# Kernel tuning notes

Hardware: AMD Instinct MI355X
Metric: run time of the kernel (lower is better)

The kernel has to match this reference:

```python
import jax, jax.numpy as jnp
import numpy as np

STATE_LEN = 128
SEQ_LEN = 2048
NUM_ITERS = 2
DIM_IN = 1024
DIM_H = 64
BATCH = 2
T_TOTAL = SEQ_LEN + 2 * STATE_LEN  # 2304
NEG = -1e30  # large-negative causal mask (avoids -inf NaNs under autodiff)


def _ln(x, g, b):
    m = jnp.mean(x, axis=-1, keepdims=True)
    v = jnp.var(x, axis=-1, keepdims=True)
    return (x - m) / jnp.sqrt(v + 1e-5) * g + b


def setup_inputs() -> dict:
    key = jax.random.key(0)
    ks = jax.random.split(key, 16)

    def w(k, fi, fo):
        # torch nn.Linear-style fan-in scaled init (keeps logits O(1))
        return jax.random.normal(k, (fi, fo), jnp.float32) / np.sqrt(fi)

    return {
        "x": jax.random.normal(ks[0], (BATCH, T_TOTAL, DIM_IN), jnp.float32),
        "Wh": w(ks[1], DIM_IN, DIM_H),
        "Whs": w(ks[2], DIM_IN, DIM_H),
        "Whe": w(ks[3], DIM_IN, DIM_H),
        "Wk": w(ks[4], DIM_H, DIM_H),
        "Wq": w(ks[5], DIM_H, DIM_H),
        "Wv": w(ks[6], DIM_H, DIM_H),
        "Wks": w(ks[7], DIM_H, DIM_H),
        "Wqs": w(ks[8], DIM_H, DIM_H),
        "Wvs": w(ks[9], DIM_H, DIM_H),
        "Wke": w(ks[10], DIM_H, DIM_H),
        "Wqe": w(ks[11], DIM_H, DIM_H),
        "Wve": w(ks[12], DIM_H, DIM_H),
        "ln_g": jnp.ones((DIM_IN,), jnp.float32),
        "ln_b": jnp.zeros((DIM_IN,), jnp.float32),
        "ln_gs": jnp.ones((DIM_IN,), jnp.float32),
        "ln_bs": jnp.zeros((DIM_IN,), jnp.float32),
        "ln_ge": jnp.ones((DIM_IN,), jnp.float32),
        "ln_be": jnp.zeros((DIM_IN,), jnp.float32),
        "cope_emb": jax.random.normal(ks[13], (DIM_H, T_TOTAL), jnp.float32),
    }


def reference(x, Wh, Whs, Whe, Wk, Wq, Wv, Wks, Wqs, Wvs, Wke, Wqe, Wve,
              ln_g, ln_b, ln_gs, ln_bs, ln_ge, ln_be, cope_emb):
    S = STATE_LEN
    # extract_state: [state_start | seq | state_end] along token dim
    xs, xm, xe = x[:, :S], x[:, S:-S], x[:, -S:]
    xm = _ln(xm, ln_g, ln_b)
    xs = _ln(xs, ln_gs, ln_bs)
    xe = _ln(xe, ln_ge, ln_be)

    mem = xm @ Wh                 # (B, L, D)
    mem_s = xs @ Whs              # (B, S, D)
    mem_e = xe @ Whe              # (B, S, D)

    scale = 1.0 / np.sqrt(DIM_H)  # xformers default scale (beta=None)
    tril = jnp.tril(jnp.ones((T_TOTAL, T_TOTAL), bool))
    mask = jnp.where(tril, 0.0, NEG)  # log of lower-triangular ones

    mem_full = None
    for ix in range(NUM_ITERS):
        k = jnp.concatenate([mem_s @ Wks, mem @ Wk, mem_e @ Wke], axis=1)  # (B,T,D)
        q = jnp.concatenate([mem_s @ Wqs, mem @ Wq, mem_e @ Wqe], axis=1)
        v = jnp.concatenate([mem_s @ Wvs, mem @ Wv, mem_e @ Wve], axis=1)

        logits = jnp.einsum('btd,bsd->bts', q, k)  # unscaled, as in CoPE gates
        if ix == 0:
            # CoPE: sigmoid-gated reverse cumsum positions + interpolated embedding bias
            gates = jax.nn.sigmoid(logits)
            pos = jnp.flip(jnp.cumsum(jnp.flip(gates, -1), axis=-1), -1)
            pos = jnp.minimum(pos, float(T_TOTAL - 1))
            pos_floor = jnp.floor(pos)
            pos_ceil = jnp.ceil(pos)
            logits_int = jnp.einsum('btd,dn->btn', q, cope_emb)  # (B,T,T)
            lc = jnp.take_along_axis(logits_int, pos_ceil.astype(jnp.int32), axis=-1)
            lf = jnp.take_along_axis(logits_int, pos_floor.astype(jnp.int32), axis=-1)
            wfrac = pos - pos_floor
            bias = lc * wfrac + lf * (1.0 - wfrac)
            scores = logits * scale + mask + bias
        else:
            scores = logits * scale + mask

        attn = jax.nn.softmax(scores, axis=-1)
        mem_full = jnp.einsum('bts,bsd->btd', attn, v)  # (B,T,D)
        if ix < NUM_ITERS - 1:
            mem_s, mem, mem_e = mem_full[:, :S], mem_full[:, S:-S], mem_full[:, -S:]
    return mem_full
```

## Files before the change

### kernel.cpp

```cpp
#include <hip/hip_runtime.h>

#define T_TOT 2304
#define S_LEN 128
#define D_IN  1024
#define D_H   64
#define BATCH 2
#define NROW  (BATCH * T_TOT)
#define CH    (T_TOT / 256)
#define SCALE 0.125f
#define KCHUNKS 8
#define KCW   (D_IN / KCHUNKS)
#define TB    16
#define FCH   288
#define NSC   8
#define NTBLK (T_TOT / TB)
#define NT16  (T_TOT / 16)
#define NPART (NSC * 4)

typedef unsigned short u16;
typedef __attribute__((ext_vector_type(8))) short short8;
typedef __attribute__((ext_vector_type(4))) float f32x4;
typedef __attribute__((ext_vector_type(4))) unsigned short u16x4;

static __device__ __forceinline__ u16 f2bf(float f) {
    unsigned u = __float_as_uint(f);
    unsigned r = (u + 0x7fffu + ((u >> 16) & 1u)) >> 16;
    return (u16)r;
}
static __device__ __forceinline__ float bf2f(u16 s) {
    return __uint_as_float((unsigned)s << 16);
}

__global__ __launch_bounds__(256) void k_ln(
    const float* __restrict__ x,
    const float* __restrict__ ln_g,  const float* __restrict__ ln_b,
    const float* __restrict__ ln_gs, const float* __restrict__ ln_bs,
    const float* __restrict__ ln_ge, const float* __restrict__ ln_be,
    u16* __restrict__ xn_hi, u16* __restrict__ xn_lo)
{
    __shared__ float red1[256], red2[256];
    const int row = blockIdx.x;
    const int t = row % T_TOT;
    const int tid = threadIdx.x;

    const float *gg, *bb;
    if (t < S_LEN)               { gg = ln_gs; bb = ln_bs; }
    else if (t >= T_TOT - S_LEN) { gg = ln_ge; bb = ln_be; }
    else                         { gg = ln_g;  bb = ln_b;  }

    const float4 xv = *(const float4*)(x + (size_t)row * D_IN + 4 * tid);
    float s  = xv.x + xv.y + xv.z + xv.w;
    float s2 = xv.x * xv.x + xv.y * xv.y + xv.z * xv.z + xv.w * xv.w;
    red1[tid] = s; red2[tid] = s2; __syncthreads();
    for (int off = 128; off > 0; off >>= 1) {
        if (tid < off) { red1[tid] += red1[tid + off]; red2[tid] += red2[tid + off]; }
        __syncthreads();
    }
    const float mean = red1[0] * (1.f / D_IN);
    const float var  = red2[0] * (1.f / D_IN) - mean * mean;
    const float rstd = rsqrtf(var + 1e-5f);

    const float4 gv = *(const float4*)(gg + 4 * tid);
    const float4 bv = *(const float4*)(bb + 4 * tid);
    float o0 = (xv.x - mean) * rstd * gv.x + bv.x;
    float o1 = (xv.y - mean) * rstd * gv.y + bv.y;
    float o2 = (xv.z - mean) * rstd * gv.z + bv.z;
    float o3 = (xv.w - mean) * rstd * gv.w + bv.w;

    u16x4 hv, lv;
    hv[0] = f2bf(o0); lv[0] = f2bf(o0 - bf2f(hv[0]));
    hv[1] = f2bf(o1); lv[1] = f2bf(o1 - bf2f(hv[1]));
    hv[2] = f2bf(o2); lv[2] = f2bf(o2 - bf2f(hv[2]));
    hv[3] = f2bf(o3); lv[3] = f2bf(o3 - bf2f(hv[3]));
    *(u16x4*)(xn_hi + (size_t)row * D_IN + 4 * tid) = hv;
    *(u16x4*)(xn_lo + (size_t)row * D_IN + 4 * tid) = lv;
}

#define WPREP_N (3 * D_H * D_IN)
__global__ __launch_bounds__(256) void k_prep(
    const float* __restrict__ Wh, const float* __restrict__ Whs, const float* __restrict__ Whe,
    const float* __restrict__ cope,
    u16* __restrict__ wT_hi, u16* __restrict__ wT_lo,
    u16* __restrict__ cT_hi, u16* __restrict__ cT_lo)
{
    const int gid = blockIdx.x * 256 + threadIdx.x;
    if (gid < WPREP_N) {
        const int seg = gid >> 16;
        const int o = gid & 65535;
        const int j = o >> 10, k = o & 1023;
        const float* W = seg == 0 ? Wh : (seg == 1 ? Whs : Whe);
        const float f = W[k * D_H + j];
        const u16 hi = f2bf(f);
        wT_hi[gid] = hi;
        wT_lo[gid] = f2bf(f - bf2f(hi));
    } else {
        const int idx = gid - WPREP_N;
        if (idx < T_TOT * D_H) {
            const int n = idx >> 6, d = idx & 63;
            const float f = cope[(size_t)d * T_TOT + n];
            const u16 hi = f2bf(f);
            cT_hi[idx] = hi;
            cT_lo[idx] = f2bf(f - bf2f(hi));
        }
    }
}

__global__ __launch_bounds__(256) void k_hgemm(
    const u16* __restrict__ xn_hi, const u16* __restrict__ xn_lo,
    const u16* __restrict__ wT_hi, const u16* __restrict__ wT_lo,
    float* __restrict__ h_part)
{
    const int tile = blockIdx.x;
    const int kc   = blockIdx.y;
    const int k0   = kc * KCW;
    const int tt = tile % 36;
    const int seg = tt < 2 ? 1 : (tt >= 34 ? 2 : 0);

    __shared__ u16 Bh[64 * KCW];
    __shared__ u16 Bl[64 * KCW];

    const int tid = threadIdx.x;
    {
        const int r = tid >> 2;
        const int c0 = (tid & 3) * 32;
        const u16* sh = wT_hi + ((size_t)seg * D_H + r) * D_IN + k0 + c0;
        const u16* sl = wT_lo + ((size_t)seg * D_H + r) * D_IN + k0 + c0;
        const int sw = (r & 7) << 3;
        #pragma unroll
        for (int u = 0; u < 4; ++u) {
            const int col = c0 + 8 * u;
            *(short8*)&Bh[r * KCW + (col ^ sw)] = *(const short8*)(sh + 8 * u);
            *(short8*)&Bl[r * KCW + (col ^ sw)] = *(const short8*)(sl + 8 * u);
        }
    }
    __syncthreads();

    const int w = tid >> 6;
    const int lane = tid & 63;
    const int l15 = lane & 15, lg4 = lane >> 4;
    const int row0 = tile * 64 + w * 16;

    const size_t abase = (size_t)(row0 + l15) * D_IN + k0 + 8 * lg4;
    f32x4 acc[4] = {};

    #pragma unroll
    for (int kk = 0; kk < KCW / 32; ++kk) {
        short8 ah = *(const short8*)(xn_hi + abase + kk * 32);
        short8 al = *(const short8*)(xn_lo + abase + kk * 32);
        #pragma unroll
        for (int j = 0; j < 4; ++j) {
            const int brow = j * 16 + l15;
            const int col = (kk * 32 + 8 * lg4) ^ ((brow & 7) << 3);
            short8 bh = *(const short8*)&Bh[brow * KCW + col];
            short8 bl = *(const short8*)&Bl[brow * KCW + col];
            acc[j] = __builtin_amdgcn_mfma_f32_16x16x32_bf16(al, bh, acc[j], 0, 0, 0);
            acc[j] = __builtin_amdgcn_mfma_f32_16x16x32_bf16(ah, bl, acc[j], 0, 0, 0);
            acc[j] = __builtin_amdgcn_mfma_f32_16x16x32_bf16(ah, bh, acc[j], 0, 0, 0);
        }
    }
    float* hp = h_part + (size_t)kc * ((size_t)NROW * D_H);
    #pragma unroll
    for (int j = 0; j < 4; ++j)
        #pragma unroll
        for (int r = 0; r < 4; ++r)
            hp[(size_t)(row0 + 4 * lg4 + r) * D_H + j * 16 + l15] = acc[j][r];
}

__global__ __launch_bounds__(256) void k_hred(
    const float* __restrict__ h_part, float* __restrict__ h)
{
    const size_t idx = (size_t)blockIdx.x * 256 + threadIdx.x;
    const size_t N = (size_t)NROW * D_H;
    float s = 0.f;
    #pragma unroll
    for (int kc = 0; kc < KCHUNKS; ++kc) s += h_part[kc * N + idx];
    h[idx] = s;
}

template <bool SPLIT>
__global__ __launch_bounds__(192) void k_qkv(
    const float* __restrict__ hin,
    const float* __restrict__ Wk,  const float* __restrict__ Wq,  const float* __restrict__ Wv,
    const float* __restrict__ Wks, const float* __restrict__ Wqs, const float* __restrict__ Wvs,
    const float* __restrict__ Wke, const float* __restrict__ Wqe, const float* __restrict__ Wve,
    u16* __restrict__ q_hi, u16* __restrict__ q_lo,
    u16* __restrict__ k_hi, u16* __restrict__ k_lo,
    u16* __restrict__ vT)
{
    __shared__ float hr[D_H];
    const int bid = blockIdx.x;
    const int b = bid / T_TOT, t = bid % T_TOT;
    const int tid = threadIdx.x;

    const float* hrow = hin + ((size_t)b * T_TOT + t) * D_H;
    if (tid < D_H) hr[tid] = hrow[tid];
    __syncthreads();

    const int which = tid >> 6, j = tid & 63;
    const float* W;
    if (t < S_LEN)               W = which == 0 ? Wks : (which == 1 ? Wqs : Wvs);
    else if (t >= T_TOT - S_LEN) W = which == 0 ? Wke : (which == 1 ? Wqe : Wve);
    else                         W = which == 0 ? Wk  : (which == 1 ? Wq  : Wv);

    float acc = 0.f;
    #pragma unroll
    for (int d = 0; d < D_H; ++d) acc += hr[d] * W[d * D_H + j];

    const size_t idx = ((size_t)b * T_TOT + t) * D_H + j;
    u16 hi = f2bf(acc);
    if (which == 0) {
        k_hi[idx] = hi;
        if (SPLIT) k_lo[idx] = f2bf(acc - bf2f(hi));
    } else if (which == 1) {
        q_hi[idx] = hi;
        if (SPLIT) q_lo[idx] = f2bf(acc - bf2f(hi));
    } else {
        vT[((size_t)b * D_H + j) * T_TOT + t] = hi;
    }
}

__global__ __launch_bounds__(256) void k_score2c(
    const u16* __restrict__ a_hi, const u16* __restrict__ a_lo,
    const u16* __restrict__ k_hi, const u16* __restrict__ k_lo,
    const u16* __restrict__ c_hi, const u16* __restrict__ c_lo,
    float* __restrict__ logits, float* __restrict__ lint,
    float* __restrict__ csum)
{
    const int b  = blockIdx.z;
    const int s0 = blockIdx.x * 64;
    const int wid = threadIdx.x >> 6;
    const int t0 = blockIdx.y * 64 + wid * 16;
    const int wt_max = t0 + 15;
    const int lane = threadIdx.x & 63;
    const int l15 = lane & 15, lg4 = lane >> 4;

    const size_t a_off = ((size_t)(b * T_TOT + t0 + l15)) * D_H + 8 * lg4;
    const short8 ah0 = *(const short8*)(a_hi + a_off);
    const short8 ah1 = *(const short8*)(a_hi + a_off + 32);
    const short8 al0 = *(const short8*)(a_lo + a_off);
    const short8 al1 = *(const short8*)(a_lo + a_off + 32);

    const size_t orow_off = ((size_t)(b * T_TOT + t0 + 4 * lg4)) * T_TOT + s0 + l15;

    {
        float* o = lint + orow_off;
        #pragma unroll
        for (int ni = 0; ni < 4; ++ni) {
            const size_t b_off = ((size_t)(s0 + ni * 16 + l15)) * D_H + 8 * lg4;
            short8 bh0 = *(const short8*)(c_hi + b_off);
            short8 bh1 = *(const short8*)(c_hi + b_off + 32);
            short8 bl0 = *(const short8*)(c_lo + b_off);
            short8 bl1 = *(const short8*)(c_lo + b_off + 32);
            f32x4 acc = {0.f, 0.f, 0.f, 0.f};
            acc = __builtin_amdgcn_mfma_f32_16x16x32_bf16(al0, bh0, acc, 0, 0, 0);
            acc = __builtin_amdgcn_mfma_f32_16x16x32_bf16(al1, bh1, acc, 0, 0, 0);
            acc = __builtin_amdgcn_mfma_f32_16x16x32_bf16(ah0, bl0, acc, 0, 0, 0);
            acc = __builtin_amdgcn_mfma_f32_16x16x32_bf16(ah1, bl1, acc, 0, 0, 0);
            acc = __builtin_amdgcn_mfma_f32_16x16x32_bf16(ah0, bh0, acc, 0, 0, 0);
            acc = __builtin_amdgcn_mfma_f32_16x16x32_bf16(ah1, bh1, acc, 0, 0, 0);
            #pragma unroll
            for (int r = 0; r < 4; ++r)
                o[(size_t)r * T_TOT + ni * 16] = acc[r];
        }
    }

    {
        const u16* bh = k_hi + (size_t)b * (T_TOT * D_H);
        const u16* bl = k_lo + (size_t)b * (T_TOT * D_H);
        float* o = logits + orow_off;
        #pragma unroll
        for (int ni = 0; ni < 4; ++ni) {
            const size_t b_off = ((size_t)(s0 + ni * 16 + l15)) * D_H + 8 * lg4;
            short8 bh0 = *(const short8*)(bh + b_off);
            short8 bh1 = *(const short8*)(bh + b_off + 32);
            short8 bl0 = *(const short8*)(bl + b_off);
            short8 bl1 = *(const short8*)(bl + b_off + 32);
            f32x4 acc = {0.f, 0.f, 0.f, 0.f};
            acc = __builtin_amdgcn_mfma_f32_16x16x32_bf16(al0, bh0, acc, 0, 0, 0);
            acc = __builtin_amdgcn_mfma_f32_16x16x32_bf16(al1, bh1, acc, 0, 0, 0);
            acc = __builtin_amdgcn_mfma_f32_16x16x32_bf16(ah0, bl0, acc, 0, 0, 0);
            acc = __builtin_amdgcn_mfma_f32_16x16x32_bf16(ah1, bl1, acc, 0, 0, 0);
            acc = __builtin_amdgcn_mfma_f32_16x16x32_bf16(ah0, bh0, acc, 0, 0, 0);
            acc = __builtin_amdgcn_mfma_f32_16x16x32_bf16(ah1, bh1, acc, 0, 0, 0);
            const int c16 = (s0 >> 4) + ni;
            #pragma unroll
            for (int r = 0; r < 4; ++r) {
                float g = 1.f / (1.f + __expf(-acc[r]));
                g += __shfl_xor(g, 1); g += __shfl_xor(g, 2);
                g += __shfl_xor(g, 4); g += __shfl_xor(g, 8);
                if (l15 == 0)
                    csum[((size_t)(b * T_TOT + t0 + 4 * lg4 + r)) * NT16 + c16] = g;
            }
            if (s0 + ni * 16 <= wt_max) {
                #pragma unroll
                for (int r = 0; r < 4; ++r)
                    o[(size_t)r * T_TOT + ni * 16] = acc[r];
            }
        }
    }
}

__global__ __launch_bounds__(256) void k_csum(
    const float* __restrict__ csum, float* __restrict__ totalv)
{
    const int row = blockIdx.x * 4 + (threadIdx.x >> 6);
    const int lane = threadIdx.x & 63;
    const size_t base = (size_t)row * NT16;
    float v = csum[base + lane] + csum[base + 64 + lane];
    if (128 + lane < NT16) v += csum[base + 128 + lane];
    #pragma unroll
    for (int off = 32; off > 0; off >>= 1) v += __shfl_xor(v, off);
    if (lane == 0) totalv[row] = v;
}

__global__ __launch_bounds__(256) void k_erow(
    const float* __restrict__ logits,
    const float* __restrict__ lint,
    const float* __restrict__ totalv,
    float* __restrict__ pbase)
{
    __shared__ float lg[T_TOT];
    __shared__ float extra[2 * T_TOT];
    __shared__ float wtot[4], wmax[4], wsum[4];

    const int row = blockIdx.x;
    const int t = row % T_TOT;
    const int Lt16 = (t | 15) + 1;
    const int Lw = min((Lt16 + 31) & ~31, T_TOT);
    const int tid = threadIdx.x;
    const int lane = tid & 63, wid = tid >> 6;
    const float* lrow = logits + (size_t)row * T_TOT;
    const float tot = totalv[row];
    const int Lc = min((int)tot + 2, T_TOT);

    for (int s = tid; s < Lt16; s += 256) lg[s] = lrow[s];
    {
        const float* lintrow = lint + (size_t)row * T_TOT;
        for (int s = tid; s < Lc; s += 256) extra[T_TOT + s] = lintrow[s];
    }
    __syncthreads();

    {
        const int base = tid * CH;
        float gv[CH];
        float lsum = 0.f;
        #pragma unroll
        for (int u = 0; u < CH; ++u) {
            const int s = base + u;
            float g = (s <= t) ? 1.f / (1.f + expf(-lg[s])) : 0.f;
            gv[u] = g;
            lsum += g;
        }
        float cs = lsum;
        #pragma unroll
        for (int off = 1; off < 64; off <<= 1) {
            float n = __shfl_up(cs, off);
            if (lane >= off) cs += n;
        }
        if (lane == 63) wtot[wid] = cs;
        __syncthreads();
        float pre = 0.f;
        #pragma unroll
        for (int w = 0; w < 4; ++w) {
            float vv = wtot[w];
            if (w < wid) pre += vv;
        }
        float run = pre + cs - lsum;
        #pragma unroll
        for (int u = 0; u < CH; ++u) {
            const int s = base + u;
            if (s <= t) {
                float p = fminf(fmaxf(tot - run, 0.f), (float)(T_TOT - 1));
                extra[s] = p;
            }
            run += gv[u];
        }
        __syncthreads();
    }

    float scv[CH];
    float mx = -3.4e38f;
    #pragma unroll
    for (int r = 0; r < CH; ++r) {
        int sidx = tid + 256 * r;
        float sc = -3.4e38f;
        if (sidx <= t) {
            sc = lg[sidx] * SCALE;
            float p = extra[sidx];
            float pf = floorf(p);
            int fi = (int)pf;
            int ci = (int)ceilf(p);
            float w = p - pf;
            sc += extra[T_TOT + ci] * w + extra[T_TOT + fi] * (1.f - w);
            mx = fmaxf(mx, sc);
        }
        scv[r] = sc;
    }
    #pragma unroll
    for (int off = 32; off > 0; off >>= 1) mx = fmaxf(mx, __shfl_xor(mx, off));
    if (lane == 0) wmax[wid] = mx;
    __syncthreads();
    mx = fmaxf(fmaxf(wmax[0], wmax[1]), fmaxf(wmax[2], wmax[3]));

    float pvv[CH];
    float psum = 0.f;
    #pragma unroll
    for (int r = 0; r < CH; ++r) {
        int sidx = tid + 256 * r;
        float pv = 0.f;
        if (sidx <= t) { pv = expf(scv[r] - mx); psum += pv; }
        pvv[r] = pv;
    }
    #pragma unroll
    for (int off = 32; off > 0; off >>= 1) psum += __shfl_xor(psum, off);
    if (lane == 0) wsum[wid] = psum;
    __syncthreads();
    const float inv = 1.f / (wsum[0] + wsum[1] + wsum[2] + wsum[3]);

    u16* prow = (u16*)(pbase + (size_t)row * T_TOT);
    #pragma unroll
    for (int r = 0; r < CH; ++r) {
        int sidx = tid + 256 * r;
        if (sidx < Lw) prow[sidx] = f2bf(pvv[r] * inv);
    }
}

__global__ __launch_bounds__(256) void k_pv(
    const float* __restrict__ pbuf, const u16* __restrict__ vT,
    float* __restrict__ opart)
{
    const int b  = blockIdx.z;
    const int scn = blockIdx.y;
    const int bx = blockIdx.x;
    const int t0 = bx * 16;
    const int sstart = scn * FCH;
    const int send = min(sstart + FCH, t0 + 16);
    if (sstart >= send) return;

    const int j0 = (threadIdx.x >> 6) * 16;
    const int lane = threadIdx.x & 63;
    const int l15 = lane & 15, lg4 = lane >> 4;

    const u16* pb = (const u16*)pbuf
        + ((size_t)(b * T_TOT + t0 + l15)) * (2 * (size_t)T_TOT) + 8 * lg4;
    const u16* vb = vT + ((size_t)(b * D_H + j0 + l15)) * T_TOT + 8 * lg4;

    f32x4 a0 = {}, a1 = {}, a2 = {}, a3 = {};
    int s = sstart;
    for (; s + 128 <= send; s += 128) {
        short8 p0 = *(const short8*)(pb + s);
        short8 v0 = *(const short8*)(vb + s);
        short8 p1 = *(const short8*)(pb + s + 32);
        short8 v1 = *(const short8*)(vb + s + 32);
        short8 p2 = *(const short8*)(pb + s + 64);
        short8 v2 = *(const short8*)(vb + s + 64);
        short8 p3 = *(const short8*)(pb + s + 96);
        short8 v3 = *(const short8*)(vb + s + 96);
        a0 = __builtin_amdgcn_mfma_f32_16x16x32_bf16(p0, v0, a0, 0, 0, 0);
        a1 = __builtin_amdgcn_mfma_f32_16x16x32_bf16(p1, v1, a1, 0, 0, 0);
        a2 = __builtin_amdgcn_mfma_f32_16x16x32_bf16(p2, v2, a2, 0, 0, 0);
        a3 = __builtin_amdgcn_mfma_f32_16x16x32_bf16(p3, v3, a3, 0, 0, 0);
    }
    for (; s < send; s += 32) {
        short8 p0 = *(const short8*)(pb + s);
        short8 v0 = *(const short8*)(vb + s);
        a0 = __builtin_amdgcn_mfma_f32_16x16x32_bf16(p0, v0, a0, 0, 0, 0);
    }
    f32x4 acc = (a0 + a1) + (a2 + a3);
    float* ob = opart + (((size_t)(b * NTBLK + bx)) * NSC + scn) * (TB * D_H)
              + (size_t)(4 * lg4) * D_H + j0 + l15;
    #pragma unroll
    for (int r = 0; r < 4; ++r) ob[(size_t)r * D_H] = acc[r];
}

__global__ __launch_bounds__(256) void k_pvmerge(
    const float* __restrict__ opart, float* __restrict__ outp)
{
    const int bid = blockIdx.x;
    const int b = bid / NTBLK, bx = bid % NTBLK;
    const int t0 = bx * 16, t_max = t0 + 15;
    const int tid = threadIdx.x;
    const int tl = tid >> 4, j4 = (tid & 15) * 4;

    float4 acc = {0.f, 0.f, 0.f, 0.f};
    for (int scn = 0; scn < NSC; ++scn) {
        if (scn * FCH <= t_max) {
            const float4 v = *(const float4*)&opart[
                (((size_t)(b * NTBLK + bx)) * NSC + scn) * (TB * D_H) + tl * D_H + j4];
            acc.x += v.x; acc.y += v.y; acc.z += v.z; acc.w += v.w;
        }
    }
    *(float4*)&outp[((size_t)(b * T_TOT + t0 + tl)) * D_H + j4] = acc;
}

__global__ __launch_bounds__(256) void k_fattn1s(
    const u16* __restrict__ q_hi, const u16* __restrict__ k_hi,
    const u16* __restrict__ vT,
    float* __restrict__ fM, float* __restrict__ fD, float* __restrict__ fO)
{
    __shared__ u16 pstage[4][TB][40];

    const int b   = blockIdx.z;
    const int scn = blockIdx.y;
    const int bx  = blockIdx.x;
    const int t0 = bx * TB;
    const int t_max = t0 + TB - 1;
    if (scn * FCH > t_max) return;

    const int tid = threadIdx.x;
    const int wid = tid >> 6;
    const int lane = tid & 63;
    const int l15 = lane & 15, lg4 = lane >> 4;

    const size_t a_off = ((size_t)(b * T_TOT + t0 + l15)) * D_H + 8 * lg4;
    const short8 ah0 = *(const short8*)(q_hi + a_off);
    const short8 ah1 = *(const short8*)(q_hi + a_off + 32);
    const u16* kh = k_hi + (size_t)b * (T_TOT * D_H);

    const int w_lo  = scn * FCH + wid * (FCH / 4);
    const int w_end = min(w_lo + FCH / 4, t_max + 1);

    float m[4]   = {-3.0e38f, -3.0e38f, -3.0e38f, -3.0e38f};
    float den[4] = {0.f, 0.f, 0.f, 0.f};
    f32x4 oacc[4] = {};

    for (int s32 = w_lo; s32 < w_end; s32 += 32) {
        f32x4 acc0 = {0.f, 0.f, 0.f, 0.f};
        f32x4 acc1 = {0.f, 0.f, 0.f, 0.f};
        const bool ir1 = (s32 + 16) < w_end;
        {
            const size_t b_off = ((size_t)(s32 + l15)) * D_H + 8 * lg4;
            short8 b0 = *(const short8*)(kh + b_off);
            short8 b1 = *(const short8*)(kh + b_off + 32);
            acc0 = __builtin_amdgcn_mfma_f32_16x16x32_bf16(ah0, b0, acc0, 0, 0, 0);
            acc0 = __builtin_amdgcn_mfma_f32_16x16x32_bf16(ah1, b1, acc0, 0, 0, 0);
        }
        if (ir1) {
            const size_t b_off = ((size_t)(s32 + 16 + l15)) * D_H + 8 * lg4;
            short8 b0 = *(const short8*)(kh + b_off);
            short8 b1 = *(const short8*)(kh + b_off + 32);
            acc1 = __builtin_amdgcn_mfma_f32_16x16x32_bf16(ah0, b0, acc1, 0, 0, 0);
            acc1 = __builtin_amdgcn_mfma_f32_16x16x32_bf16(ah1, b1, acc1, 0, 0, 0);
        }
        #pragma unroll
        for (int r = 0; r < 4; ++r) {
            const int tl = 4 * lg4 + r;
            const int c0 = s32 + l15, c1 = s32 + 16 + l15;
            const bool v0 = (c0 < w_end) && (c0 <= t0 + tl);
            const bool v1 = ir1 && (c1 < w_end) && (c1 <= t0 + tl);
            const float sc0 = acc0[r] * SCALE;
            const float sc1 = acc1[r] * SCALE;
            float tmx = fmaxf(v0 ? sc0 : -3.0e38f, v1 ? sc1 : -3.0e38f);
            tmx = fmaxf(tmx, __shfl_xor(tmx, 1));
            tmx = fmaxf(tmx, __shfl_xor(tmx, 2));
            tmx = fmaxf(tmx, __shfl_xor(tmx, 4));
            tmx = fmaxf(tmx, __shfl_xor(tmx, 8));
            const float mn = fmaxf(m[r], tmx);
            const float scl = __expf(m[r] - mn);
            m[r] = mn;
            const float p0 = v0 ? __expf(sc0 - mn) : 0.f;
            const float p1 = v1 ? __expf(sc1 - mn) : 0.f;
            float ps = p0 + p1;
            ps += __shfl_xor(ps, 1); ps += __shfl_xor(ps, 2);
            ps += __shfl_xor(ps, 4); ps += __shfl_xor(ps, 8);
            den[r] = den[r] * scl + ps;
            #pragma unroll
            for (int j = 0; j < 4; ++j) oacc[j][r] *= scl;
            pstage[wid][tl][l15] = f2bf(p0);
            pstage[wid][tl][16 + l15] = f2bf(p1);
        }
        const short8 pa = *(const short8*)&pstage[wid][l15][8 * lg4];
        #pragma unroll
        for (int j = 0; j < 4; ++j) {
            const size_t v_off = ((size_t)(b * D_H + j * 16 + l15)) * T_TOT + s32 + 8 * lg4;
            short8 bv = *(const short8*)(vT + v_off);
            oacc[j] = __builtin_amdgcn_mfma_f32_16x16x32_bf16(pa, bv, oacc[j], 0, 0, 0);
        }
    }

    const size_t pidx = ((size_t)(b * NTBLK + bx)) * NPART + scn * 4 + wid;
    if (l15 == 0) {
        #pragma unroll
        for (int r = 0; r < 4; ++r) {
            fM[pidx * TB + 4 * lg4 + r] = m[r];
            fD[pidx * TB + 4 * lg4 + r] = den[r];
        }
    }
    #pragma unroll
    for (int j = 0; j < 4; ++j)
        #pragma unroll
        for (int r = 0; r < 4; ++r)
            fO[pidx * (TB * D_H) + (size_t)(4 * lg4 + r) * D_H + j * 16 + l15] = oacc[j][r];
}

__global__ __launch_bounds__(256) void k_fmerge(
    const float* __restrict__ fM, const float* __restrict__ fD,
    const float* __restrict__ fO, float* __restrict__ outp)
{
    const int bid = blockIdx.x;
    const int b = bid / NTBLK, bx = bid % NTBLK;
    const int t0 = bx * 16, t_max = t0 + 15;
    const int tid = threadIdx.x;
    const int tl = tid >> 4, j4 = (tid & 15) * 4;
    const size_t pb = (size_t)bid * NPART;

    float M = -3.0e38f;
    #pragma unroll
    for (int c = 0; c < NPART; ++c)
        if ((c >> 2) * FCH <= t_max) M = fmaxf(M, fM[(pb + c) * TB + tl]);

    float D = 0.f;
    float4 O = {0.f, 0.f, 0.f, 0.f};
    for (int c = 0; c < NPART; ++c) {
        if ((c >> 2) * FCH <= t_max) {
            const float w = __expf(fM[(pb + c) * TB + tl] - M);
            D += w * fD[(pb + c) * TB + tl];
            const float4 ov = *(const float4*)&fO[(pb + c) * (TB * D_H) + tl * D_H + j4];
            O.x += w * ov.x; O.y += w * ov.y; O.z += w * ov.z; O.w += w * ov.w;
        }
    }
    const float inv = 1.f / D;
    float4 res; res.x = O.x * inv; res.y = O.y * inv; res.z = O.z * inv; res.w = O.w * inv;
    *(float4*)&outp[((size_t)(b * T_TOT + t0 + tl)) * D_H + j4] = res;
}

extern "C" void kernel_launch(void* const* d_in, const int* in_sizes, int n_in,
                              void* d_out, int out_size, void* d_ws, size_t ws_size,
                              hipStream_t stream) {
    const float* x    = (const float*)d_in[0];
    const float* Wh   = (const float*)d_in[1];
    const float* Whs  = (const float*)d_in[2];
    const float* Whe  = (const float*)d_in[3];
    const float* Wk   = (const float*)d_in[4];
    const float* Wq   = (const float*)d_in[5];
    const float* Wv   = (const float*)d_in[6];
    const float* Wks  = (const float*)d_in[7];
    const float* Wqs  = (const float*)d_in[8];
    const float* Wvs  = (const float*)d_in[9];
    const float* Wke  = (const float*)d_in[10];
    const float* Wqe  = (const float*)d_in[11];
    const float* Wve  = (const float*)d_in[12];
    const float* ln_g  = (const float*)d_in[13];
    const float* ln_b  = (const float*)d_in[14];
    const float* ln_gs = (const float*)d_in[15];
    const float* ln_bs = (const float*)d_in[16];
    const float* ln_ge = (const float*)d_in[17];
    const float* ln_be = (const float*)d_in[18];
    const float* cope  = (const float*)d_in[19];

    float* out = (float*)d_out;

    const size_t N = (size_t)NROW * D_H;
    char* W = (char*)d_ws;
    u16* xn_hi  = (u16*)W;    W += (size_t)NROW * D_IN * 2;
    u16* xn_lo  = (u16*)W;    W += (size_t)NROW * D_IN * 2;
    u16* wT_hi  = (u16*)W;    W += (size_t)3 * D_H * D_IN * 2;
    u16* wT_lo  = (u16*)W;    W += (size_t)3 * D_H * D_IN * 2;
    float* h    = (float*)W;  W += N * 4;
    u16* q_hi   = (u16*)W;    W += N * 2;
    u16* q_lo   = (u16*)W;    W += N * 2;
    u16* k_hi   = (u16*)W;    W += N * 2;
    u16* k_lo   = (u16*)W;    W += N * 2;
    u16* vT     = (u16*)W;    W += N * 2;
    u16* cT_hi  = (u16*)W;    W += (size_t)T_TOT * D_H * 2;
    u16* cT_lo  = (u16*)W;    W += (size_t)T_TOT * D_H * 2;
    float* logits = (float*)W; W += (size_t)BATCH * T_TOT * T_TOT * 4;
    float* lint   = (float*)W; W += (size_t)BATCH * T_TOT * T_TOT * 4;
    float* csum   = (float*)W; W += (size_t)NROW * NT16 * 4;
    float* totalv = (float*)W; W += (size_t)NROW * 4;
    float* mem1   = (float*)W; W += N * 4;
    float* opart  = (float*)W; W += (size_t)BATCH * NTBLK * NSC * TB * D_H * 4;
    float* fM     = (float*)W; W += (size_t)BATCH * NTBLK * NPART * TB * 4;
    float* fD     = (float*)W; W += (size_t)BATCH * NTBLK * NPART * TB * 4;
    float* fO     = (float*)W; W += (size_t)BATCH * NTBLK * NPART * TB * D_H * 4;

    float* h_part = lint;

    k_ln<<<NROW, 256, 0, stream>>>(x, ln_g, ln_b, ln_gs, ln_bs, ln_ge, ln_be,
                                   xn_hi, xn_lo);
    k_prep<<<(WPREP_N + T_TOT * D_H + 255) / 256, 256, 0, stream>>>(
        Wh, Whs, Whe, cope, wT_hi, wT_lo, cT_hi, cT_lo);
    k_hgemm<<<dim3(NROW / 64, KCHUNKS), 256, 0, stream>>>(xn_hi, xn_lo, wT_hi, wT_lo, h_part);
    k_hred<<<(int)(N / 256), 256, 0, stream>>>(h_part, h);

    k_qkv<true><<<NROW, 192, 0, stream>>>(h, Wk, Wq, Wv, Wks, Wqs, Wvs, Wke, Wqe, Wve,
                                          q_hi, q_lo, k_hi, k_lo, vT);
    k_score2c<<<dim3(T_TOT / 64, T_TOT / 64, BATCH), 256, 0, stream>>>(
        q_hi, q_lo, k_hi, k_lo, cT_hi, cT_lo, logits, lint, csum);
    k_csum<<<NROW / 4, 256, 0, stream>>>(csum, totalv);
    k_erow<<<NROW, 256, 0, stream>>>(logits, lint, totalv, lint);
    k_pv<<<dim3(NTBLK, NSC, BATCH), 256, 0, stream>>>(lint, vT, opart);
    k_pvmerge<<<BATCH * NTBLK, 256, 0, stream>>>(opart, mem1);

    k_qkv<false><<<NROW, 192, 0, stream>>>(mem1, Wk, Wq, Wv, Wks, Wqs, Wvs, Wke, Wqe, Wve,
                                           q_hi, q_lo, k_hi, k_lo, vT);
    k_fattn1s<<<dim3(NTBLK, NSC, BATCH), 256, 0, stream>>>(q_hi, k_hi, vT, fM, fD, fO);
    k_fmerge<<<BATCH * NTBLK, 256, 0, stream>>>(fM, fD, fO, out);
}
```

Before: 194.7 us.

## Split CoPE interpolation GEMM out and bound it by total gate sum

```diff
diff --git a/kernel.cpp b/kernel.cpp
--- a/kernel.cpp
+++ b/kernel.cpp
@@ -219,12 +219,10 @@
     }
 }
 
-__global__ __launch_bounds__(256) void k_score2c(
+__global__ __launch_bounds__(256) void k_gatesl(
     const u16* __restrict__ a_hi, const u16* __restrict__ a_lo,
     const u16* __restrict__ k_hi, const u16* __restrict__ k_lo,
-    const u16* __restrict__ c_hi, const u16* __restrict__ c_lo,
-    float* __restrict__ logits, float* __restrict__ lint,
-    float* __restrict__ csum)
+    float* __restrict__ logits, float* __restrict__ csum)
 {
     const int b  = blockIdx.z;
     const int s0 = blockIdx.x * 64;
@@ -240,62 +238,37 @@
     const short8 al0 = *(const short8*)(a_lo + a_off);
     const short8 al1 = *(const short8*)(a_lo + a_off + 32);
 
-    const size_t orow_off = ((size_t)(b * T_TOT + t0 + 4 * lg4)) * T_TOT + s0 + l15;
-
-    {
-        float* o = lint + orow_off;
-        #pragma unroll
-        for (int ni = 0; ni < 4; ++ni) {
-            const size_t b_off = ((size_t)(s0 + ni * 16 + l15)) * D_H + 8 * lg4;
-            short8 bh0 = *(const short8*)(c_hi + b_off);
-            short8 bh1 = *(const short8*)(c_hi + b_off + 32);
-            short8 bl0 = *(const short8*)(c_lo + b_off);
-            short8 bl1 = *(const short8*)(c_lo + b_off + 32);
-            f32x4 acc = {0.f, 0.f, 0.f, 0.f};
-            acc = __builtin_amdgcn_mfma_f32_16x16x32_bf16(al0, bh0, acc, 0, 0, 0);
-            acc = __builtin_amdgcn_mfma_f32_16x16x32_bf16(al1, bh1, acc, 0, 0, 0);
-            acc = __builtin_amdgcn_mfma_f32_16x16x32_bf16(ah0, bl0, acc, 0, 0, 0);
-            acc = __builtin_amdgcn_mfma_f32_16x16x32_bf16(ah1, bl1, acc, 0, 0, 0);
-            acc = __builtin_amdgcn_mfma_f32_16x16x32_bf16(ah0, bh0, acc, 0, 0, 0);
-            acc = __builtin_amdgcn_mfma_f32_16x16x32_bf16(ah1, bh1, acc, 0, 0, 0);
+    const u16* bh = k_hi + (size_t)b * (T_TOT * D_H);
+    const u16* bl = k_lo + (size_t)b * (T_TOT * D_H);
+    float* o = logits + ((size_t)(b * T_TOT + t0 + 4 * lg4)) * T_TOT + s0 + l15;
+
+    #pragma unroll
+    for (int ni = 0; ni < 4; ++ni) {
+        const size_t b_off = ((size_t)(s0 + ni * 16 + l15)) * D_H + 8 * lg4;
+        short8 bh0 = *(const short8*)(bh + b_off);
+        short8 bh1 = *(const short8*)(bh + b_off + 32);
+        short8 bl0 = *(const short8*)(bl + b_off);
+        short8 bl1 = *(const short8*)(bl + b_off + 32);
+        f32x4 acc = {0.f, 0.f, 0.f, 0.f};
+        acc = __builtin_amdgcn_mfma_f32_16x16x32_bf16(al0, bh0, acc, 0, 0, 0);
+        acc = __builtin_amdgcn_mfma_f32_16x16x32_bf16(al1, bh1, acc, 0, 0, 0);
+        acc = __builtin_amdgcn_mfma_f32_16x16x32_bf16(ah0, bl0, acc, 0, 0, 0);
+        acc = __builtin_amdgcn_mfma_f32_16x16x32_bf16(ah1, bl1, acc, 0, 0, 0);
+        acc = __builtin_amdgcn_mfma_f32_16x16x32_bf16(ah0, bh0, acc, 0, 0, 0);
+        acc = __builtin_amdgcn_mfma_f32_16x16x32_bf16(ah1, bh1, acc, 0, 0, 0);
+        const int c16 = (s0 >> 4) + ni;
+        #pragma unroll
+        for (int r = 0; r < 4; ++r) {
+            float g = 1.f / (1.f + __expf(-acc[r]));
+            g += __shfl_xor(g, 1); g += __shfl_xor(g, 2);
+            g += __shfl_xor(g, 4); g += __shfl_xor(g, 8);
+            if (l15 == 0)
+                csum[((size_t)(b * T_TOT + t0 + 4 * lg4 + r)) * NT16 + c16] = g;
+        }
+        if (s0 + ni * 16 <= wt_max) {
             #pragma unroll
             for (int r = 0; r < 4; ++r)
                 o[(size_t)r * T_TOT + ni * 16] = acc[r];
-        }
-    }
-
-    {
-        const u16* bh = k_hi + (size_t)b * (T_TOT * D_H);
-        const u16* bl = k_lo + (size_t)b * (T_TOT * D_H);
-        float* o = logits + orow_off;
-        #pragma unroll
-        for (int ni = 0; ni < 4; ++ni) {
-            const size_t b_off = ((size_t)(s0 + ni * 16 + l15)) * D_H + 8 * lg4;
-            short8 bh0 = *(const short8*)(bh + b_off);
-            short8 bh1 = *(const short8*)(bh + b_off + 32);
-            short8 bl0 = *(const short8*)(bl + b_off);
-            short8 bl1 = *(const short8*)(bl + b_off + 32);
-            f32x4 acc = {0.f, 0.f, 0.f, 0.f};
-            acc = __builtin_amdgcn_mfma_f32_16x16x32_bf16(al0, bh0, acc, 0, 0, 0);
-            acc = __builtin_amdgcn_mfma_f32_16x16x32_bf16(al1, bh1, acc, 0, 0, 0);
-            acc = __builtin_amdgcn_mfma_f32_16x16x32_bf16(ah0, bl0, acc, 0, 0, 0);
-            acc = __builtin_amdgcn_mfma_f32_16x16x32_bf16(ah1, bl1, acc, 0, 0, 0);
-            acc = __builtin_amdgcn_mfma_f32_16x16x32_bf16(ah0, bh0, acc, 0, 0, 0);
-            acc = __builtin_amdgcn_mfma_f32_16x16x32_bf16(ah1, bh1, acc, 0, 0, 0);
-            const int c16 = (s0 >> 4) + ni;
-            #pragma unroll
-            for (int r = 0; r < 4; ++r) {
-                float g = 1.f / (1.f + __expf(-acc[r]));
-                g += __shfl_xor(g, 1); g += __shfl_xor(g, 2);
-                g += __shfl_xor(g, 4); g += __shfl_xor(g, 8);
-                if (l15 == 0)
-                    csum[((size_t)(b * T_TOT + t0 + 4 * lg4 + r)) * NT16 + c16] = g;
-            }
-            if (s0 + ni * 16 <= wt_max) {
-                #pragma unroll
-                for (int r = 0; r < 4; ++r)
-                    o[(size_t)r * T_TOT + ni * 16] = acc[r];
-            }
         }
     }
 }
@@ -311,6 +284,55 @@
     #pragma unroll
     for (int off = 32; off > 0; off >>= 1) v += __shfl_xor(v, off);
     if (lane == 0) totalv[row] = v;
+}
+
+__global__ __launch_bounds__(256) void k_lintb(
+    const u16* __restrict__ a_hi, const u16* __restrict__ a_lo,
+    const u16* __restrict__ c_hi, const u16* __restrict__ c_lo,
+    const float* __restrict__ totalv,
+    float* __restrict__ lint)
+{
+    const int b  = blockIdx.z;
+    const int s0 = blockIdx.x * 64;
+    const int wid = threadIdx.x >> 6;
+    const int t0 = blockIdx.y * 64 + wid * 16;
+    const int lane = threadIdx.x & 63;
+    const int l15 = lane & 15, lg4 = lane >> 4;
+
+    float tv = totalv[b * T_TOT + t0 + l15];
+    tv = fmaxf(tv, __shfl_xor(tv, 1));
+    tv = fmaxf(tv, __shfl_xor(tv, 2));
+    tv = fmaxf(tv, __shfl_xor(tv, 4));
+    tv = fmaxf(tv, __shfl_xor(tv, 8));
+    const int bound = min((int)tv + 2, T_TOT);
+    if (s0 >= bound) return;
+
+    const size_t a_off = ((size_t)(b * T_TOT + t0 + l15)) * D_H + 8 * lg4;
+    const short8 ah0 = *(const short8*)(a_hi + a_off);
+    const short8 ah1 = *(const short8*)(a_hi + a_off + 32);
+    const short8 al0 = *(const short8*)(a_lo + a_off);
+    const short8 al1 = *(const short8*)(a_lo + a_off + 32);
+
+    float* o = lint + ((size_t)(b * T_TOT + t0 + 4 * lg4)) * T_TOT + s0 + l15;
+
+    #pragma unroll
+    for (int ni = 0; ni < 4; ++ni) {
+        const size_t b_off = ((size_t)(s0 + ni * 16 + l15)) * D_H + 8 * lg4;
+        short8 bh0 = *(const short8*)(c_hi + b_off);
+        short8 bh1 = *(const short8*)(c_hi + b_off + 32);
+        short8 bl0 = *(const short8*)(c_lo + b_off);
+        short8 bl1 = *(const short8*)(c_lo + b_off + 32);
+        f32x4 acc = {0.f, 0.f, 0.f, 0.f};
+        acc = __builtin_amdgcn_mfma_f32_16x16x32_bf16(al0, bh0, acc, 0, 0, 0);
+        acc = __builtin_amdgcn_mfma_f32_16x16x32_bf16(al1, bh1, acc, 0, 0, 0);
+        acc = __builtin_amdgcn_mfma_f32_16x16x32_bf16(ah0, bl0, acc, 0, 0, 0);
+        acc = __builtin_amdgcn_mfma_f32_16x16x32_bf16(ah1, bl1, acc, 0, 0, 0);
+        acc = __builtin_amdgcn_mfma_f32_16x16x32_bf16(ah0, bh0, acc, 0, 0, 0);
+        acc = __builtin_amdgcn_mfma_f32_16x16x32_bf16(ah1, bh1, acc, 0, 0, 0);
+        #pragma unroll
+        for (int r = 0; r < 4; ++r)
+            o[(size_t)r * T_TOT + ni * 16] = acc[r];
+    }
 }
 
 __global__ __launch_bounds__(256) void k_erow(
@@ -685,9 +707,11 @@
 
     k_qkv<true><<<NROW, 192, 0, stream>>>(h, Wk, Wq, Wv, Wks, Wqs, Wvs, Wke, Wqe, Wve,
                                           q_hi, q_lo, k_hi, k_lo, vT);
-    k_score2c<<<dim3(T_TOT / 64, T_TOT / 64, BATCH), 256, 0, stream>>>(
-        q_hi, q_lo, k_hi, k_lo, cT_hi, cT_lo, logits, lint, csum);
+    k_gatesl<<<dim3(T_TOT / 64, T_TOT / 64, BATCH), 256, 0, stream>>>(
+        q_hi, q_lo, k_hi, k_lo, logits, csum);
     k_csum<<<NROW / 4, 256, 0, stream>>>(csum, totalv);
+    k_lintb<<<dim3(T_TOT / 64, T_TOT / 64, BATCH), 256, 0, stream>>>(
+        q_hi, q_lo, cT_hi, cT_lo, totalv, lint);
     k_erow<<<NROW, 256, 0, stream>>>(logits, lint, totalv, lint);
     k_pv<<<dim3(NTBLK, NSC, BATCH), 256, 0, stream>>>(lint, vT, opart);
     k_pvmerge<<<BATCH * NTBLK, 256, 0, stream>>>(opart, mem1);
```

Measured after the change: 193.4 us. About the same (-0.7%).
